# Kernel optimization log

Hardware: AMD Instinct MI355X
Metric: run time of the kernel (lower is better)

Reference implementation:

```python
import jax, jax.numpy as jnp
import numpy as np

N_NODES = 150000
N_EDGES = 2400000
IN_DIM, HID, OUT_DIM = 2, 32, 1


def gcn_conv(x, edge_index, W, b, n_nodes):
    """PyG-style GCNConv: add self-loops, sym-normalize, aggregate, linear."""
    h = x @ W  # [N, F_out] linear first (as in PyG GCNConv)
    loop = jnp.arange(n_nodes)
    src = jnp.concatenate([edge_index[0], loop])
    dst = jnp.concatenate([edge_index[1], loop])
    deg = jax.ops.segment_sum(jnp.ones(src.shape[0], h.dtype), dst,
                              num_segments=n_nodes)  # in-degree incl. self-loops
    dinv = jnp.where(deg > 0, jax.lax.rsqrt(deg), 0.0)
    norm = dinv[src] * dinv[dst]  # [E+N]
    msg = h[src] * norm[:, None]  # gather + scale
    out = jax.ops.segment_sum(msg, dst, num_segments=n_nodes)  # scatter-add
    return out + b


def setup_inputs() -> dict:
    key = jax.random.key(0)
    ks = jax.random.split(key, 8)
    x = jax.random.normal(ks[0], (N_NODES, IN_DIM), dtype=jnp.float32)
    edge_index = jax.random.randint(ks[1], (2, N_EDGES), 0, N_NODES, dtype=jnp.int32)
    W1 = jax.random.normal(ks[2], (IN_DIM, HID), dtype=jnp.float32) / np.sqrt(IN_DIM)
    b1 = jnp.zeros((HID,), jnp.float32)
    W2 = jax.random.normal(ks[3], (HID, HID), dtype=jnp.float32) / np.sqrt(HID)
    b2 = jnp.zeros((HID,), jnp.float32)
    Wp = jax.random.normal(ks[4], (HID, OUT_DIM), dtype=jnp.float32) / np.sqrt(HID)
    bp = jnp.zeros((OUT_DIM,), jnp.float32)
    return {"x": x, "edge_index": edge_index, "W1": W1, "b1": b1,
            "W2": W2, "b2": b2, "Wp": Wp, "bp": bp}


def reference(x, edge_index, W1, b1, W2, b2, Wp, bp):
    n = x.shape[0]
    h = jax.nn.relu(gcn_conv(x, edge_index, W1, b1, n))
    h = jax.nn.relu(gcn_conv(h, edge_index, W2, b2, n))
    return jax.nn.sigmoid(h @ Wp + bp)  # [N, 1]
```

## Files before the change

### kernel.cpp

```cpp
#include <hip/hip_runtime.h>

#define HID 32
#define SH 9
#define BNODES 512
#define NBMAX 320
#define TILE 8192
#define CAP 16384
#define STAGECAP 12288

typedef unsigned int uint;

__device__ __forceinline__ uint f2bf(float v) {
    uint b = __float_as_uint(v);
    return (b + 0x7fffu + ((b >> 16) & 1u)) >> 16;
}

__global__ void k_zero(int* __restrict__ p, int n) {
    int i = blockIdx.x * 256 + threadIdx.x;
    if (i < n) p[i] = 0;
}

__global__ void __launch_bounds__(512) k_bucketize(
        const int* __restrict__ src, const int* __restrict__ dst,
        int* __restrict__ bcur, uint* __restrict__ ebuf, int E, int NB) {
    __shared__ uint  ecache[TILE];
    __shared__ unsigned short bcache[TILE];
    __shared__ int cnt[NBMAX];
    __shared__ int loff[NBMAX + 1];
    __shared__ int gbase[NBMAX];
    int tid = threadIdx.x;
    int tbase = blockIdx.x * TILE;
    int tcount = min(E - tbase, TILE);
    int tc4 = tcount >> 2;
    const int4* dst4 = (const int4*)(dst + tbase);
    const int4* src4 = (const int4*)(src + tbase);

    for (int b = tid; b < NBMAX; b += 512) cnt[b] = 0;
    __syncthreads();
#pragma unroll
    for (int k = 0; k < TILE / 4 / 512; ++k) {
        int q = k * 512 + tid;
        if (q < tc4) {
            int4 d = dst4[q];
            atomicAdd(&cnt[d.x >> SH], 1);
            atomicAdd(&cnt[d.y >> SH], 1);
            atomicAdd(&cnt[d.z >> SH], 1);
            atomicAdd(&cnt[d.w >> SH], 1);
        }
    }
    if (tid == 0)
        for (int t = tc4 << 2; t < tcount; ++t) atomicAdd(&cnt[dst[tbase + t] >> SH], 1);
    __syncthreads();
    if (tid < 64) {
        int lo = tid * 5;
        int s = 0;
        for (int b = lo; b < lo + 5 && b < NB; ++b) s += cnt[b];
        int v = s;
        for (int off = 1; off < 64; off <<= 1) {
            int u = __shfl_up(v, off, 64);
            if (tid >= off) v += u;
        }
        int excl = v - s;
        for (int b = lo; b < lo + 5 && b < NB; ++b) { loff[b] = excl; excl += cnt[b]; }
        if (tid == 63) loff[NB] = excl;
    }
    __syncthreads();
    for (int b = tid; b < NB; b += 512) cnt[b] = loff[b];
    __syncthreads();
#pragma unroll
    for (int k = 0; k < TILE / 4 / 512; ++k) {
        int q = k * 512 + tid;
        if (q < tc4) {
            int4 d = dst4[q];
            int4 s = src4[q];
            int b0 = d.x >> SH, p0 = atomicAdd(&cnt[b0], 1);
            ecache[p0] = (uint)s.x | ((uint)(d.x & (BNODES - 1)) << 18); bcache[p0] = (unsigned short)b0;
            int b1 = d.y >> SH, p1_ = atomicAdd(&cnt[b1], 1);
            ecache[p1_] = (uint)s.y | ((uint)(d.y & (BNODES - 1)) << 18); bcache[p1_] = (unsigned short)b1;
            int b2 = d.z >> SH, p2_ = atomicAdd(&cnt[b2], 1);
            ecache[p2_] = (uint)s.z | ((uint)(d.z & (BNODES - 1)) << 18); bcache[p2_] = (unsigned short)b2;
            int b3 = d.w >> SH, p3_ = atomicAdd(&cnt[b3], 1);
            ecache[p3_] = (uint)s.w | ((uint)(d.w & (BNODES - 1)) << 18); bcache[p3_] = (unsigned short)b3;
        }
    }
    if (tid == 0)
        for (int t = tc4 << 2; t < tcount; ++t) {
            int d = dst[tbase + t];
            int b_ = d >> SH;
            int pos = atomicAdd(&cnt[b_], 1);
            ecache[pos] = (uint)src[tbase + t] | ((uint)(d & (BNODES - 1)) << 18);
            bcache[pos] = (unsigned short)b_;
        }
    __syncthreads();
    for (int b = tid; b < NB; b += 512) {
        int tc = loff[b + 1] - loff[b];
        if (tc > 0) gbase[b] = b * CAP + atomicAdd(&bcur[b], tc);
    }
    __syncthreads();
    for (int j = tid; j < tcount; j += 512) {
        int b = bcache[j];
        ebuf[gbase[b] + (j - loff[b])] = ecache[j];
    }
}

__global__ void k_scanb(const int* __restrict__ bcur, int* __restrict__ bbase,
                        int* __restrict__ rowptr, int N, int NB) {
    __shared__ int l[NBMAX + 1];
    int tid = threadIdx.x;
    if (tid < 64) {
        int lo = tid * 5;
        int s = 0;
        for (int b = lo; b < lo + 5 && b < NB; ++b) s += bcur[b];
        int v = s;
        for (int off = 1; off < 64; off <<= 1) {
            int u = __shfl_up(v, off, 64);
            if (tid >= off) v += u;
        }
        int excl = v - s;
        for (int b = lo; b < lo + 5 && b < NB; ++b) { l[b] = excl; excl += bcur[b]; }
        if (tid == 63) l[NB] = excl;
    }
    __syncthreads();
    for (int b = tid; b <= NB; b += blockDim.x) bbase[b] = l[b];
    if (tid == 0) rowptr[N] = l[NB];
}

__global__ void __launch_bounds__(512) k_sortb(
        const uint* __restrict__ ebuf, const int* __restrict__ bcur,
        const int* __restrict__ bbase, const float* __restrict__ x,
        int* __restrict__ rowptr, float* __restrict__ dinv,
        float2* __restrict__ p1, int* __restrict__ col, int N) {
    __shared__ int c[BNODES];
    __shared__ int off[BNODES];
    __shared__ int cur[BNODES];
    __shared__ uint stage[STAGECAP];
    int b = blockIdx.x, tid = threadIdx.x;
    int cnt = bcur[b];
    const uint* eb = ebuf + (long)b * CAP;
    int cbase = bbase[b];
    for (int t = tid; t < BNODES; t += 512) c[t] = 0;
    __syncthreads();
    int vc = cnt >> 2;
    const uint4* e4 = (const uint4*)eb;
    for (int q = tid; q < vc; q += 512) {
        uint4 e = e4[q];
        atomicAdd(&c[e.x >> 18], 1);
        atomicAdd(&c[e.y >> 18], 1);
        atomicAdd(&c[e.z >> 18], 1);
        atomicAdd(&c[e.w >> 18], 1);
        int j = q << 2;
        if (j + 3 < STAGECAP) {
            stage[j] = e.x; stage[j + 1] = e.y; stage[j + 2] = e.z; stage[j + 3] = e.w;
        }
    }
    for (int j = (vc << 2) + tid; j < cnt; j += 512) {
        uint e = eb[j];
        atomicAdd(&c[e >> 18], 1);
        if (j < STAGECAP) stage[j] = e;
    }
    __syncthreads();
    if (tid < 64) {
        int lo = tid * 8, s = 0;
#pragma unroll
        for (int k = 0; k < 8; ++k) s += c[lo + k];
        int v = s;
        for (int o = 1; o < 64; o <<= 1) {
            int u = __shfl_up(v, o, 64);
            if (tid >= o) v += u;
        }
        int excl = v - s;
#pragma unroll
        for (int k = 0; k < 8; ++k) { off[lo + k] = excl; excl += c[lo + k]; }
    }
    __syncthreads();
    for (int t = tid; t < BNODES; t += 512) {
        cur[t] = off[t];
        int node = (b << SH) + t;
        if (node < N) {
            rowptr[node] = cbase + off[t];
            float di = rsqrtf((float)c[t] + 1.0f);
            dinv[node] = di;
            float2 xv = ((const float2*)x)[node];
            p1[node] = make_float2(xv.x * di, xv.y * di);
        }
    }
    __syncthreads();
    int lim = min(cnt, STAGECAP);
    for (int j = tid; j < lim; j += 512) {
        uint e = stage[j];
        int dl = e >> 18;
        int pos = atomicAdd(&cur[dl], 1);
        col[cbase + pos] = (int)(e & 0x3FFFF);
    }
    for (int j = STAGECAP + tid; j < cnt; j += 512) {
        uint e = eb[j];
        int dl = e >> 18;
        int pos = atomicAdd(&cur[dl], 1);
        col[cbase + pos] = (int)(e & 0x3FFFF);
    }
}

__global__ void __launch_bounds__(256) k_gl12(
        const int* __restrict__ rowptr, const int* __restrict__ col,
        const float2* __restrict__ p1, const float* __restrict__ dinv,
        const float* __restrict__ W1, const float* __restrict__ b1,
        const float* __restrict__ W2, uint* __restrict__ p2h, int N) {
    __shared__ float sW1[64], sb1[32], sW2[HID * HID];
    int tid = threadIdx.x;
    for (int t = tid; t < HID * HID; t += 256) sW2[t] = W2[t];
    if (tid < 64) sW1[tid] = W1[tid];
    if (tid < 32) sb1[tid] = b1[tid];
    __syncthreads();
    int i = blockIdx.x * 16 + (tid >> 4);
    if (i >= N) return;
    int sub = tid & 15;

    int beg = rowptr[i], end = rowptr[i + 1];
    float ax = 0, ay = 0, bx = 0, by = 0;
    int j = beg + sub;
    for (; j + 16 < end; j += 32) {
        int c0 = col[j], c1 = col[j + 16];
        float2 v0 = p1[c0], v1 = p1[c1];
        ax += v0.x; ay += v0.y;
        bx += v1.x; by += v1.y;
    }
    if (j < end) {
        float2 v = p1[col[j]];
        ax += v.x; ay += v.y;
    }
    float sx = ax + bx, sy = ay + by;
#pragma unroll
    for (int m = 1; m < 16; m <<= 1) {
        sx += __shfl_xor(sx, m, 16);
        sy += __shfl_xor(sy, m, 16);
    }

    float2 a = p1[i];
    float di = dinv[i];
    float g0 = di * (a.x + sx);
    float g1 = di * (a.y + sy);

    float h0 = fmaxf(g0 * sW1[2 * sub] + g1 * sW1[32 + 2 * sub] + sb1[2 * sub], 0.0f);
    float h1 = fmaxf(g0 * sW1[2 * sub + 1] + g1 * sW1[32 + 2 * sub + 1] + sb1[2 * sub + 1], 0.0f);

    float o0 = 0, o1 = 0;
    int fb = 2 * sub;
#pragma unroll
    for (int s = 0; s < 16; ++s) {
        float hk0 = __shfl(h0, s, 16);
        float hk1 = __shfl(h1, s, 16);
        const float* w0 = &sW2[(2 * s) * HID + fb];
        const float* w1 = &sW2[(2 * s + 1) * HID + fb];
        o0 += hk0 * w0[0]; o1 += hk0 * w0[1];
        o0 += hk1 * w1[0]; o1 += hk1 * w1[1];
    }

    p2h[(long)i * 16 + sub] = f2bf(di * o0) | (f2bf(di * o1) << 16);
}

__global__ void k_gout(const int* __restrict__ rowptr, const int* __restrict__ col,
                       const uint* __restrict__ p2h, const float* __restrict__ b2,
                       const float* __restrict__ Wp, const float* __restrict__ bp,
                       const float* __restrict__ dinv, float* __restrict__ out, int N) {
    int node = blockIdx.x * 16 + (threadIdx.x >> 4);
    if (node >= N) return;
    int hl = threadIdx.x & 15;
    int beg = rowptr[node], end = rowptr[node + 1];
    uint w = p2h[(long)node * 16 + hl];
    float sA0 = __uint_as_float(w << 16), sB0 = __uint_as_float(w & 0xffff0000u);
    float sA1 = 0, sB1 = 0, sA2 = 0, sB2 = 0, sA3 = 0, sB3 = 0;
    int j = beg;
    for (; j + 4 <= end; j += 4) {
        int c0 = col[j], c1 = col[j + 1], c2 = col[j + 2], c3 = col[j + 3];
        uint w0 = p2h[(long)c0 * 16 + hl];
        uint w1 = p2h[(long)c1 * 16 + hl];
        uint w2 = p2h[(long)c2 * 16 + hl];
        uint w3 = p2h[(long)c3 * 16 + hl];
        sA0 += __uint_as_float(w0 << 16); sB0 += __uint_as_float(w0 & 0xffff0000u);
        sA1 += __uint_as_float(w1 << 16); sB1 += __uint_as_float(w1 & 0xffff0000u);
        sA2 += __uint_as_float(w2 << 16); sB2 += __uint_as_float(w2 & 0xffff0000u);
        sA3 += __uint_as_float(w3 << 16); sB3 += __uint_as_float(w3 & 0xffff0000u);
    }
    for (; j < end; ++j) {
        uint wj = p2h[(long)col[j] * 16 + hl];
        sA0 += __uint_as_float(wj << 16); sB0 += __uint_as_float(wj & 0xffff0000u);
    }
    float sA = (sA0 + sA1) + (sA2 + sA3);
    float sB = (sB0 + sB1) + (sB2 + sB3);
    float di = dinv[node];
    float hvA = fmaxf(di * sA + b2[2 * hl], 0.0f);
    float hvB = fmaxf(di * sB + b2[2 * hl + 1], 0.0f);
    float v = hvA * Wp[2 * hl] + hvB * Wp[2 * hl + 1];
#pragma unroll
    for (int m = 8; m > 0; m >>= 1) v += __shfl_xor(v, m, 16);
    if (hl == 0) out[node] = 1.0f / (1.0f + expf(-(v + bp[0])));
}

extern "C" void kernel_launch(void* const* d_in, const int* in_sizes, int n_in,
                              void* d_out, int out_size, void* d_ws, size_t ws_size,
                              hipStream_t stream) {
    const float* x  = (const float*)d_in[0];
    const int*   ei = (const int*)d_in[1];
    const float* W1 = (const float*)d_in[2];
    const float* b1 = (const float*)d_in[3];
    const float* W2 = (const float*)d_in[4];
    const float* b2 = (const float*)d_in[5];
    const float* Wp = (const float*)d_in[6];
    const float* bp = (const float*)d_in[7];
    float* out = (float*)d_out;

    const int N = in_sizes[0] / 2;
    const int E = in_sizes[1] / 2;
    const int* src = ei;
    const int* dst = ei + E;
    const int NB = (N + BNODES - 1) >> SH;

    char* ws = (char*)d_ws;
    size_t off = 0;
    auto alloc = [&](size_t bytes) {
        void* ptr = ws + off;
        off += (bytes + 255) & ~(size_t)255;
        return ptr;
    };
    int*    bcur   = (int*)alloc((size_t)NBMAX * 4);
    int*    bbase  = (int*)alloc((size_t)(NBMAX + 1) * 4);
    int*    rowptr = (int*)alloc((size_t)(N + 1) * 4);
    float*  dinv   = (float*)alloc((size_t)N * 4);
    uint*   ebuf   = (uint*)alloc((size_t)NBMAX * CAP * 4);
    int*    col    = (int*)alloc((size_t)E * 4);
    float2* p1     = (float2*)alloc((size_t)N * 8);
    uint*   p2h    = (uint*)alloc((size_t)N * 16 * 4);

    const int nb_t = (E + TILE - 1) / TILE;
    const int nb_g = (N + 15) / 16;

    k_zero<<<(NBMAX + 255) / 256, 256, 0, stream>>>(bcur, NBMAX);
    k_bucketize<<<nb_t, 512, 0, stream>>>(src, dst, bcur, ebuf, E, NB);
    k_scanb<<<1, 256, 0, stream>>>(bcur, bbase, rowptr, N, NB);
    k_sortb<<<NB, 512, 0, stream>>>(ebuf, bcur, bbase, x, rowptr, dinv, p1, col, N);
    k_gl12<<<nb_g, 256, 0, stream>>>(rowptr, col, p1, dinv, W1, b1, W2, p2h, N);
    k_gout<<<nb_g, 256, 0, stream>>>(rowptr, col, p2h, b2, Wp, bp, dinv, out, N);
}
```

Before: 120.6 us.

## Split layer-2 feature table into two halves gathered in separate passes

The bf16 layer-2 feature table is split into two 32-byte-per-node arrays, and the final aggregation runs as two passes, one per feature half. The first pass stores a partial projection and the second combines it and applies the sigmoid. Each pass gathers from a table half the size (2.4 MB instead of 4.8 MB), which is meant to raise cache hit rates for the random neighbour gathers. The cost is reading the CSR column indices twice, an extra launch, and a partial-sum buffer.

After: 134.8 us. 11.8% more time.

```diff
diff --git a/kernel.cpp b/kernel.cpp
--- a/kernel.cpp
+++ b/kernel.cpp
@@ -204,7 +204,8 @@
         const int* __restrict__ rowptr, const int* __restrict__ col,
         const float2* __restrict__ p1, const float* __restrict__ dinv,
         const float* __restrict__ W1, const float* __restrict__ b1,
-        const float* __restrict__ W2, uint* __restrict__ p2h, int N) {
+        const float* __restrict__ W2, uint* __restrict__ p2a,
+        uint* __restrict__ p2b, int N) {
     __shared__ float sW1[64], sb1[32], sW2[HID * HID];
     int tid = threadIdx.x;
     for (int t = tid; t < HID * HID; t += 256) sW2[t] = W2[t];
@@ -255,45 +256,54 @@
         o0 += hk1 * w1[0]; o1 += hk1 * w1[1];
     }
 
-    p2h[(long)i * 16 + sub] = f2bf(di * o0) | (f2bf(di * o1) << 16);
-}
-
-__global__ void k_gout(const int* __restrict__ rowptr, const int* __restrict__ col,
-                       const uint* __restrict__ p2h, const float* __restrict__ b2,
-                       const float* __restrict__ Wp, const float* __restrict__ bp,
-                       const float* __restrict__ dinv, float* __restrict__ out, int N) {
-    int node = blockIdx.x * 16 + (threadIdx.x >> 4);
+    uint word = f2bf(di * o0) | (f2bf(di * o1) << 16);
+    if (sub < 8) p2a[(long)i * 8 + sub] = word;
+    else         p2b[(long)i * 8 + (sub - 8)] = word;
+}
+
+template <int HALF>
+__global__ void __launch_bounds__(256) k_gouth(
+        const int* __restrict__ rowptr, const int* __restrict__ col,
+        const uint* __restrict__ px, const float* __restrict__ b2,
+        const float* __restrict__ Wp, const float* __restrict__ bp,
+        const float* __restrict__ dinv, float* __restrict__ vpart,
+        float* __restrict__ out, int N) {
+    int node = blockIdx.x * 32 + (threadIdx.x >> 3);
     if (node >= N) return;
-    int hl = threadIdx.x & 15;
+    int sl = threadIdx.x & 7;
     int beg = rowptr[node], end = rowptr[node + 1];
-    uint w = p2h[(long)node * 16 + hl];
+    uint w = px[(long)node * 8 + sl];
     float sA0 = __uint_as_float(w << 16), sB0 = __uint_as_float(w & 0xffff0000u);
     float sA1 = 0, sB1 = 0, sA2 = 0, sB2 = 0, sA3 = 0, sB3 = 0;
     int j = beg;
     for (; j + 4 <= end; j += 4) {
         int c0 = col[j], c1 = col[j + 1], c2 = col[j + 2], c3 = col[j + 3];
-        uint w0 = p2h[(long)c0 * 16 + hl];
-        uint w1 = p2h[(long)c1 * 16 + hl];
-        uint w2 = p2h[(long)c2 * 16 + hl];
-        uint w3 = p2h[(long)c3 * 16 + hl];
+        uint w0 = px[(long)c0 * 8 + sl];
+        uint w1 = px[(long)c1 * 8 + sl];
+        uint w2 = px[(long)c2 * 8 + sl];
+        uint w3 = px[(long)c3 * 8 + sl];
         sA0 += __uint_as_float(w0 << 16); sB0 += __uint_as_float(w0 & 0xffff0000u);
         sA1 += __uint_as_float(w1 << 16); sB1 += __uint_as_float(w1 & 0xffff0000u);
         sA2 += __uint_as_float(w2 << 16); sB2 += __uint_as_float(w2 & 0xffff0000u);
         sA3 += __uint_as_float(w3 << 16); sB3 += __uint_as_float(w3 & 0xffff0000u);
     }
     for (; j < end; ++j) {
-        uint wj = p2h[(long)col[j] * 16 + hl];
+        uint wj = px[(long)col[j] * 8 + sl];
         sA0 += __uint_as_float(wj << 16); sB0 += __uint_as_float(wj & 0xffff0000u);
     }
     float sA = (sA0 + sA1) + (sA2 + sA3);
     float sB = (sB0 + sB1) + (sB2 + sB3);
     float di = dinv[node];
-    float hvA = fmaxf(di * sA + b2[2 * hl], 0.0f);
-    float hvB = fmaxf(di * sB + b2[2 * hl + 1], 0.0f);
-    float v = hvA * Wp[2 * hl] + hvB * Wp[2 * hl + 1];
-#pragma unroll
-    for (int m = 8; m > 0; m >>= 1) v += __shfl_xor(v, m, 16);
-    if (hl == 0) out[node] = 1.0f / (1.0f + expf(-(v + bp[0])));
+    int f0 = 16 * HALF + 2 * sl;
+    float hvA = fmaxf(di * sA + b2[f0], 0.0f);
+    float hvB = fmaxf(di * sB + b2[f0 + 1], 0.0f);
+    float v = hvA * Wp[f0] + hvB * Wp[f0 + 1];
+#pragma unroll
+    for (int m = 4; m > 0; m >>= 1) v += __shfl_xor(v, m, 8);
+    if (sl == 0) {
+        if (HALF == 0) vpart[node] = v;
+        else out[node] = 1.0f / (1.0f + expf(-(v + vpart[node] + bp[0])));
+    }
 }
 
 extern "C" void kernel_launch(void* const* d_in, const int* in_sizes, int n_in,
@@ -329,15 +339,19 @@
     uint*   ebuf   = (uint*)alloc((size_t)NBMAX * CAP * 4);
     int*    col    = (int*)alloc((size_t)E * 4);
     float2* p1     = (float2*)alloc((size_t)N * 8);
-    uint*   p2h    = (uint*)alloc((size_t)N * 16 * 4);
+    uint*   p2a    = (uint*)alloc((size_t)N * 8 * 4);
+    uint*   p2b    = (uint*)alloc((size_t)N * 8 * 4);
+    float*  vpart  = (float*)alloc((size_t)N * 4);
 
     const int nb_t = (E + TILE - 1) / TILE;
     const int nb_g = (N + 15) / 16;
+    const int nb_h = (N + 31) / 32;
 
     k_zero<<<(NBMAX + 255) / 256, 256, 0, stream>>>(bcur, NBMAX);
     k_bucketize<<<nb_t, 512, 0, stream>>>(src, dst, bcur, ebuf, E, NB);
     k_scanb<<<1, 256, 0, stream>>>(bcur, bbase, rowptr, N, NB);
     k_sortb<<<NB, 512, 0, stream>>>(ebuf, bcur, bbase, x, rowptr, dinv, p1, col, N);
-    k_gl12<<<nb_g, 256, 0, stream>>>(rowptr, col, p1, dinv, W1, b1, W2, p2h, N);
-    k_gout<<<nb_g, 256, 0, stream>>>(rowptr, col, p2h, b2, Wp, bp, dinv, out, N);
-}
+    k_gl12<<<nb_g, 256, 0, stream>>>(rowptr, col, p1, dinv, W1, b1, W2, p2a, p2b, N);
+    k_gouth<0><<<nb_h, 256, 0, stream>>>(rowptr, col, p2a, b2, Wp, bp, dinv, vpart, out, N);
+    k_gouth<1><<<nb_h, 256, 0, stream>>>(rowptr, col, p2b, b2, Wp, bp, dinv, vpart, out, N);
+}
```
